# Kernel optimization log

Hardware: AMD Instinct MI355X
Metric: run time of the kernel (lower is better)

The kernel has to match this reference:

```python
import jax, jax.numpy as jnp
import numpy as np

N_NODES = 50000
N_EDGES = 800000
IN_DIM = 128
HID = 64
HEADS = 2
OUT_DIM = 2
N_GRAPHS = 512
NEG_SLOPE = 0.2


def setup_inputs() -> dict:
    key = jax.random.key(0)
    ks = jax.random.split(key, 16)
    x = jax.random.normal(ks[0], (N_NODES, IN_DIM), dtype=jnp.float32)
    edge_index = jax.random.randint(ks[1], (2, N_EDGES), 0, N_NODES, dtype=jnp.int64)
    batch = jnp.sort(jax.random.randint(ks[2], (N_NODES,), 0, N_GRAPHS, dtype=jnp.int64))
    s = 0.1
    W1 = jax.random.normal(ks[3], (IN_DIM, HEADS * HID), dtype=jnp.float32) * s
    a_src1 = jax.random.normal(ks[4], (HEADS, HID), dtype=jnp.float32) * s
    a_dst1 = jax.random.normal(ks[5], (HEADS, HID), dtype=jnp.float32) * s
    b1 = jnp.zeros((HEADS * HID,), dtype=jnp.float32)
    W2 = jax.random.normal(ks[6], (HEADS * HID, HID), dtype=jnp.float32) * s
    a_src2 = jax.random.normal(ks[7], (1, HID), dtype=jnp.float32) * s
    a_dst2 = jax.random.normal(ks[8], (1, HID), dtype=jnp.float32) * s
    b2 = jnp.zeros((HID,), dtype=jnp.float32)
    fcW = jax.random.normal(ks[9], (HID, OUT_DIM), dtype=jnp.float32) * s
    fcb = jnp.zeros((OUT_DIM,), dtype=jnp.float32)
    return dict(x=x, edge_index=edge_index, batch=batch,
                W1=W1, a_src1=a_src1, a_dst1=a_dst1, b1=b1,
                W2=W2, a_src2=a_src2, a_dst2=a_dst2, b2=b2,
                fcW=fcW, fcb=fcb)


def gat_layer(x, src, dst, W, a_src, a_dst, b, heads, c_out):
    # x: [N, F] -> h: [N, H, C]
    N = x.shape[0]
    h = (x @ W).reshape(N, heads, c_out)
    alpha_s = jnp.sum(h * a_src, axis=-1)  # [N, H]
    alpha_d = jnp.sum(h * a_dst, axis=-1)  # [N, H]
    e = jax.nn.leaky_relu(alpha_s[src] + alpha_d[dst], NEG_SLOPE)  # [E, H]
    # segment softmax over destination nodes
    emax = jax.ops.segment_max(e, dst, num_segments=N)  # [N, H]
    ex = jnp.exp(e - emax[dst])
    denom = jax.ops.segment_sum(ex, dst, num_segments=N)  # [N, H]
    coef = ex / denom[dst]  # [E, H]
    msg = h[src] * coef[..., None]  # [E, H, C]
    out = jax.ops.segment_sum(msg, dst, num_segments=N)  # [N, H, C]
    return out.reshape(N, heads * c_out) + b


def reference(x, edge_index, batch, W1, a_src1, a_dst1, b1, W2, a_src2, a_dst2, b2, fcW, fcb):
    N = x.shape[0]
    # PyG GATConv add_self_loops=True (shared graph for both layers)
    loops = jnp.arange(N, dtype=edge_index.dtype)
    src = jnp.concatenate([edge_index[0], loops])
    dst = jnp.concatenate([edge_index[1], loops])
    h = jax.nn.relu(gat_layer(x, src, dst, W1, a_src1, a_dst1, b1, HEADS, HID))
    h = jax.nn.relu(gat_layer(h, src, dst, W2, a_src2, a_dst2, b2, 1, HID))
    # global mean pool over graphs
    sums = jax.ops.segment_sum(h, batch, num_segments=N_GRAPHS)  # [G, HID]
    cnts = jax.ops.segment_sum(jnp.ones((N,), dtype=h.dtype), batch, num_segments=N_GRAPHS)
    pooled = sums / jnp.maximum(cnts, 1.0)[:, None]
    logits = pooled @ fcW + fcb
    return jax.nn.log_softmax(logits, axis=1)
```

## Files before the change

### kernel.cpp

```cpp
#include <hip/hip_runtime.h>
#include <math.h>

#define N_NODES 50000
#define N_EDGES 800000
#define EP (N_EDGES + N_NODES)
#define IN_DIM 128
#define HID 64
#define HEADS 2
#define OUT_DIM 2
#define N_GRAPHS 512
#define NEG_SLOPE 0.2f
#define NB_SCAN 196

typedef unsigned int uint;
typedef unsigned short ushort;

__device__ __forceinline__ ushort f2bf(float f) {
    uint u = __float_as_uint(f);
    u += 0x7fffu + ((u >> 16) & 1u);
    return (ushort)(u >> 16);
}
__device__ __forceinline__ float bf_lo(uint u) { return __uint_as_float(u << 16); }
__device__ __forceinline__ float bf_hi(uint u) { return __uint_as_float(u & 0xffff0000u); }

__global__ void hist_kernel(const int* __restrict__ ei, int* __restrict__ cnt) {
    int i = blockIdx.x * blockDim.x + threadIdx.x;
    if (i >= EP) return;
    int d = (i < N_EDGES) ? ei[N_EDGES + i] : (i - N_EDGES);
    atomicAdd(&cnt[d], 1);
}

__global__ void partial_kernel(const int* __restrict__ cnt, int* __restrict__ bsum) {
    int tid = threadIdx.x;
    int i = blockIdx.x * 256 + tid;
    int lane = tid & 63, wid = tid >> 6;
    int v = (i < N_NODES) ? cnt[i] : 0;
#pragma unroll
    for (int off = 32; off; off >>= 1) v += __shfl_xor(v, off);
    __shared__ int wsum[4];
    if (lane == 0) wsum[wid] = v;
    __syncthreads();
    if (tid == 0) bsum[blockIdx.x] = wsum[0] + wsum[1] + wsum[2] + wsum[3];
}

__global__ void scanb_kernel(const int* __restrict__ bsum, int* __restrict__ boff,
                             int* __restrict__ rowptr) {
    int tid = threadIdx.x;
    int lane = tid & 63, wid = tid >> 6;
    int v = (tid < NB_SCAN) ? bsum[tid] : 0;
    int incl = v;
#pragma unroll
    for (int off = 1; off < 64; off <<= 1) {
        int t = __shfl_up(incl, off);
        if (lane >= off) incl += t;
    }
    __shared__ int wt[4];
    if (lane == 63) wt[wid] = incl;
    __syncthreads();
    int add = 0;
    for (int w = 0; w < wid; w++) add += wt[w];
    incl += add;
    if (tid < NB_SCAN) boff[tid] = incl - v;
    if (tid == NB_SCAN - 1) rowptr[N_NODES] = incl;
}

__global__ void scanc_kernel(const int* __restrict__ cnt, const int* __restrict__ boff,
                             int* __restrict__ rowptr, int* __restrict__ cursor) {
    int tid = threadIdx.x;
    int i = blockIdx.x * 256 + tid;
    int lane = tid & 63, wid = tid >> 6;
    int v = (i < N_NODES) ? cnt[i] : 0;
    int incl = v;
#pragma unroll
    for (int off = 1; off < 64; off <<= 1) {
        int t = __shfl_up(incl, off);
        if (lane >= off) incl += t;
    }
    __shared__ int wt[4];
    if (lane == 63) wt[wid] = incl;
    __syncthreads();
    int add = boff[blockIdx.x];
    for (int w = 0; w < wid; w++) add += wt[w];
    int excl = add + incl - v;
    if (i < N_NODES) { rowptr[i] = excl; cursor[i] = excl; }
}

__global__ void scatter_kernel(const int* __restrict__ ei, int* __restrict__ cursor,
                               int* __restrict__ csr_src) {
    int i = blockIdx.x * blockDim.x + threadIdx.x;
    if (i >= EP) return;
    int s, d;
    if (i < N_EDGES) { s = ei[i]; d = ei[N_EDGES + i]; }
    else             { s = d = i - N_EDGES; }
    int pos = atomicAdd(&cursor[d], 1);
    csr_src[pos] = s;
}

template<int K, int COLS, int NPB>
__global__ void gemm_nodes(const float* __restrict__ X, const float* __restrict__ W,
                           ushort* __restrict__ Y, int n_nodes) {
    __shared__ float xs[NPB][K];
    const int base = blockIdx.x * NPB;
    const int tid = threadIdx.x;
    const float4* X4 = (const float4*)X;
    for (int idx = tid; idx < NPB * (K / 4); idx += COLS) {
        int r = idx / (K / 4), c = idx % (K / 4);
        int n = base + r;
        float4 v = (n < n_nodes) ? X4[(size_t)n * (K / 4) + c] : make_float4(0.f, 0.f, 0.f, 0.f);
        ((float4*)xs[r])[c] = v;
    }
    __syncthreads();
    float acc[NPB];
#pragma unroll
    for (int i = 0; i < NPB; i++) acc[i] = 0.f;
    for (int k = 0; k < K; k++) {
        float w = W[(size_t)k * COLS + tid];
#pragma unroll
        for (int i = 0; i < NPB; i++) acc[i] = fmaf(xs[i][k], w, acc[i]);
    }
#pragma unroll
    for (int i = 0; i < NPB; i++) {
        int n = base + i;
        if (n < n_nodes) Y[(size_t)n * COLS + tid] = f2bf(acc[i]);
    }
}

template<int H>
__global__ void alphas_kernel(const uint* __restrict__ Hb,
                              const float* __restrict__ a_src,
                              const float* __restrict__ a_dst,
                              float* __restrict__ as, float* __restrict__ ad, int n) {
    int i = blockIdx.x * blockDim.x + threadIdx.x;
    if (i >= n) return;
    const uint* hp = Hb + (size_t)i * (H * 32);
#pragma unroll
    for (int h = 0; h < H; h++) {
        float s = 0.f, d = 0.f;
#pragma unroll 8
        for (int j = 0; j < 32; j++) {
            uint u = hp[h * 32 + j];
            float v0 = bf_lo(u), v1 = bf_hi(u);
            s = fmaf(v0, a_src[h * 64 + 2 * j], s);
            s = fmaf(v1, a_src[h * 64 + 2 * j + 1], s);
            d = fmaf(v0, a_dst[h * 64 + 2 * j], d);
            d = fmaf(v1, a_dst[h * 64 + 2 * j + 1], d);
        }
        as[(size_t)i * H + h] = s;
        ad[(size_t)i * H + h] = d;
    }
}

__device__ __forceinline__ float lrelu(float e) { return e > 0.f ? e : NEG_SLOPE * e; }

__global__ void node_agg1_kernel(const int* __restrict__ rowptr, const int* __restrict__ csr_src,
                                 const uint* __restrict__ Hb,
                                 const float* __restrict__ as, const float* __restrict__ ad,
                                 const float* __restrict__ b, float* __restrict__ outp,
                                 float* __restrict__ exbuf) {
    int wave = threadIdx.x >> 6;
    int lane = threadIdx.x & 63;
    int node = blockIdx.x * 4 + wave;
    if (node >= N_NODES) return;
    const int lo = rowptr[node], hi = rowptr[node + 1];
    const float ad0 = ad[(size_t)node * 2 + 0], ad1 = ad[(size_t)node * 2 + 1];

    float d0 = 0.f, d1 = 0.f;
    for (int j = lo + lane; j < hi; j += 64) {
        int s = csr_src[j];
        float2 a = *(const float2*)&as[(size_t)s * 2];
        float ex0 = __expf(lrelu(a.x + ad0));
        float ex1 = __expf(lrelu(a.y + ad1));
        *(float2*)&exbuf[(size_t)j * 2] = make_float2(ex0, ex1);
        d0 += ex0; d1 += ex1;
    }
#pragma unroll
    for (int off = 32; off; off >>= 1) {
        d0 += __shfl_xor(d0, off);
        d1 += __shfl_xor(d1, off);
    }
    const float inv = (lane < 32) ? (1.f / d0) : (1.f / d1);

    float acc0 = 0.f, acc1 = 0.f;
    int j = lo;
    for (; j + 4 <= hi; j += 4) {
        int s0 = csr_src[j + 0], s1 = csr_src[j + 1];
        int s2 = csr_src[j + 2], s3 = csr_src[j + 3];
        float2 e0 = *(const float2*)&exbuf[(size_t)(j + 0) * 2];
        float2 e1 = *(const float2*)&exbuf[(size_t)(j + 1) * 2];
        float2 e2 = *(const float2*)&exbuf[(size_t)(j + 2) * 2];
        float2 e3 = *(const float2*)&exbuf[(size_t)(j + 3) * 2];
        uint u0 = Hb[(size_t)s0 * 64 + lane];
        uint u1 = Hb[(size_t)s1 * 64 + lane];
        uint u2 = Hb[(size_t)s2 * 64 + lane];
        uint u3 = Hb[(size_t)s3 * 64 + lane];
        float c0 = (lane < 32) ? e0.x : e0.y;
        float c1 = (lane < 32) ? e1.x : e1.y;
        float c2 = (lane < 32) ? e2.x : e2.y;
        float c3 = (lane < 32) ? e3.x : e3.y;
        acc0 = fmaf(bf_lo(u0), c0, acc0); acc1 = fmaf(bf_hi(u0), c0, acc1);
        acc0 = fmaf(bf_lo(u1), c1, acc0); acc1 = fmaf(bf_hi(u1), c1, acc1);
        acc0 = fmaf(bf_lo(u2), c2, acc0); acc1 = fmaf(bf_hi(u2), c2, acc1);
        acc0 = fmaf(bf_lo(u3), c3, acc0); acc1 = fmaf(bf_hi(u3), c3, acc1);
    }
    for (; j < hi; j++) {
        int s = csr_src[j];
        float2 e = *(const float2*)&exbuf[(size_t)j * 2];
        uint u = Hb[(size_t)s * 64 + lane];
        float c = (lane < 32) ? e.x : e.y;
        acc0 = fmaf(bf_lo(u), c, acc0);
        acc1 = fmaf(bf_hi(u), c, acc1);
    }
    float v0 = acc0 * inv + b[2 * lane];
    float v1 = acc1 * inv + b[2 * lane + 1];
    v0 = v0 > 0.f ? v0 : 0.f;
    v1 = v1 > 0.f ? v1 : 0.f;
    *(float2*)&outp[(size_t)node * 128 + 2 * lane] = make_float2(v0, v1);
}

__global__ void node_agg2_kernel(const int* __restrict__ rowptr, const int* __restrict__ csr_src,
                                 const ushort* __restrict__ Hb,
                                 const float* __restrict__ as, const float* __restrict__ ad,
                                 const float* __restrict__ b, float* __restrict__ outp,
                                 float* __restrict__ exbuf) {
    int wave = threadIdx.x >> 6;
    int lane = threadIdx.x & 63;
    int node = blockIdx.x * 4 + wave;
    if (node >= N_NODES) return;
    const int lo = rowptr[node], hi = rowptr[node + 1];
    const float adN = ad[node];

    float d = 0.f;
    for (int j = lo + lane; j < hi; j += 64) {
        float ex = __expf(lrelu(as[csr_src[j]] + adN));
        exbuf[j] = ex;
        d += ex;
    }
#pragma unroll
    for (int off = 32; off; off >>= 1) d += __shfl_xor(d, off);
    const float inv = 1.f / d;

    float acc = 0.f;
    int j = lo;
    for (; j + 4 <= hi; j += 4) {
        int s0 = csr_src[j + 0], s1 = csr_src[j + 1];
        int s2 = csr_src[j + 2], s3 = csr_src[j + 3];
        float e0 = exbuf[j + 0], e1 = exbuf[j + 1];
        float e2 = exbuf[j + 2], e3 = exbuf[j + 3];
        float h0 = __uint_as_float(((uint)Hb[(size_t)s0 * 64 + lane]) << 16);
        float h1 = __uint_as_float(((uint)Hb[(size_t)s1 * 64 + lane]) << 16);
        float h2 = __uint_as_float(((uint)Hb[(size_t)s2 * 64 + lane]) << 16);
        float h3 = __uint_as_float(((uint)Hb[(size_t)s3 * 64 + lane]) << 16);
        acc = fmaf(h0, e0, acc);
        acc = fmaf(h1, e1, acc);
        acc = fmaf(h2, e2, acc);
        acc = fmaf(h3, e3, acc);
    }
    for (; j < hi; j++)
        acc = fmaf(__uint_as_float(((uint)Hb[(size_t)csr_src[j] * 64 + lane]) << 16),
                   exbuf[j], acc);
    float v = acc * inv + b[lane];
    outp[(size_t)node * 64 + lane] = v > 0.f ? v : 0.f;
}

__global__ void pool_fc_kernel(const float* __restrict__ act2,
                               const int* __restrict__ batch,
                               const float* __restrict__ fcW,
                               const float* __restrict__ fcb,
                               float* __restrict__ out) {
    int g = blockIdx.x;
    int tid = threadIdx.x;
    int wid = tid >> 6, c = tid & 63;
    __shared__ int slo, shi;
    if (tid == 0) {
        int lo = 0, hi = N_NODES;
        while (lo < hi) { int m = (lo + hi) >> 1; if (batch[m] < g) lo = m + 1; else hi = m; }
        slo = lo;
        lo = 0; hi = N_NODES;
        while (lo < hi) { int m = (lo + hi) >> 1; if (batch[m] < g + 1) lo = m + 1; else hi = m; }
        shi = lo;
    }
    __syncthreads();
    const int lo = slo, hi = shi;
    float sum = 0.f;
    for (int n = lo + wid; n < hi; n += 4) sum += act2[(size_t)n * HID + c];
    __shared__ float ps[4][HID];
    ps[wid][c] = sum;
    __syncthreads();
    if (wid == 0) {
        float t = ps[0][c] + ps[1][c] + ps[2][c] + ps[3][c];
        float cnt = (float)(hi - lo);
        __shared__ float pooled[HID];
        pooled[c] = t / fmaxf(cnt, 1.f);
        __syncthreads();
        __shared__ float ls[OUT_DIM];
        if (c < OUT_DIM) {
            float l = fcb[c];
#pragma unroll 8
            for (int k = 0; k < HID; k++) l = fmaf(pooled[k], fcW[k * OUT_DIM + c], l);
            ls[c] = l;
        }
        __syncthreads();
        if (c < OUT_DIM) {
            float m = fmaxf(ls[0], ls[1]);
            float lse = m + logf(expf(ls[0] - m) + expf(ls[1] - m));
            out[(size_t)g * OUT_DIM + c] = ls[c] - lse;
        }
    }
}

extern "C" void kernel_launch(void* const* d_in, const int* in_sizes, int n_in,
                              void* d_out, int out_size, void* d_ws, size_t ws_size,
                              hipStream_t stream) {
    const float* x    = (const float*)d_in[0];
    const int*   ei   = (const int*)d_in[1];
    const int*   batch= (const int*)d_in[2];
    const float* W1   = (const float*)d_in[3];
    const float* as1w = (const float*)d_in[4];
    const float* ad1w = (const float*)d_in[5];
    const float* b1   = (const float*)d_in[6];
    const float* W2   = (const float*)d_in[7];
    const float* as2w = (const float*)d_in[8];
    const float* ad2w = (const float*)d_in[9];
    const float* b2   = (const float*)d_in[10];
    const float* fcW  = (const float*)d_in[11];
    const float* fcb  = (const float*)d_in[12];

    const size_t N = N_NODES;
    float* ws = (float*)d_ws;
    ushort* h1b  = (ushort*)ws;
    float* act1  = ws + N * 64;
    ushort* h2b  = (ushort*)(act1 + N * 128);
    float* out2  = act1 + N * 128 + N * 32;
    float* alps1 = out2 + N * 64;
    float* alpd1 = alps1 + N * 2;
    float* alps2 = alpd1 + N * 2;
    float* alpd2 = alps2 + N;
    int* cnt     = (int*)(alpd2 + N);
    int* rowptr  = cnt + N;
    int* cursor  = rowptr + N + 1;
    int* bsum    = cursor + N;
    int* boff    = bsum + NB_SCAN;
    int* csr_src = boff + NB_SCAN;
    float* exbuf = (float*)(csr_src + EP);

    hipMemsetAsync(cnt, 0, N * sizeof(int), stream);
    hist_kernel<<<(EP + 255) / 256, 256, 0, stream>>>(ei, cnt);
    partial_kernel<<<NB_SCAN, 256, 0, stream>>>(cnt, bsum);
    scanb_kernel<<<1, 256, 0, stream>>>(bsum, boff, rowptr);
    scanc_kernel<<<NB_SCAN, 256, 0, stream>>>(cnt, boff, rowptr, cursor);
    scatter_kernel<<<(EP + 255) / 256, 256, 0, stream>>>(ei, cursor, csr_src);

    gemm_nodes<128, 128, 4><<<(N + 3) / 4, 128, 0, stream>>>(x, W1, h1b, (int)N);
    alphas_kernel<2><<<(N + 255) / 256, 256, 0, stream>>>((const uint*)h1b, as1w, ad1w, alps1, alpd1, (int)N);
    node_agg1_kernel<<<(N + 3) / 4, 256, 0, stream>>>(rowptr, csr_src, (const uint*)h1b, alps1, alpd1, b1, act1, exbuf);

    gemm_nodes<128, 64, 8><<<(N + 7) / 8, 64, 0, stream>>>(act1, W2, h2b, (int)N);
    alphas_kernel<1><<<(N + 255) / 256, 256, 0, stream>>>((const uint*)h2b, as2w, ad2w, alps2, alpd2, (int)N);
    node_agg2_kernel<<<(N + 3) / 4, 256, 0, stream>>>(rowptr, csr_src, h2b, alps2, alpd2, b2, out2, exbuf);

    pool_fc_kernel<<<N_GRAPHS, 256, 0, stream>>>(out2, batch, fcW, fcb, (float*)d_out);
}
```

Measured before the change: 355.5 us.

## Fuse attention-logit dot products into GEMM and keep edge exps in registers

The separate alphas kernels are folded into the node GEMM: each wave multiplies its fp32 accumulators by a_src/a_dst and reduces them with a wave shuffle, so the bf16 features are not read back and two launches disappear. In both aggregation kernels the per-edge exp values are no longer written to and re-read from a global exbuf. For the first 128 edges of each node they stay in registers and are broadcast with __shfl, and edges beyond 128 recompute the exp. The alphas now come from unrounded fp32 accumulators rather than bf16 values, which slightly changes numerics. The GEMM epilogue gains a shuffle reduction per node.

```diff
diff --git a/kernel.cpp b/kernel.cpp
--- a/kernel.cpp
+++ b/kernel.cpp
@@ -96,12 +96,15 @@
     csr_src[pos] = s;
 }
 
-template<int K, int COLS, int NPB>
-__global__ void gemm_nodes(const float* __restrict__ X, const float* __restrict__ W,
-                           ushort* __restrict__ Y, int n_nodes) {
+template<int K, int COLS, int NPB, int H>
+__global__ void gemm_alphas(const float* __restrict__ X, const float* __restrict__ W,
+                            ushort* __restrict__ Y,
+                            const float* __restrict__ a_src, const float* __restrict__ a_dst,
+                            float* __restrict__ as, float* __restrict__ ad, int n_nodes) {
     __shared__ float xs[NPB][K];
     const int base = blockIdx.x * NPB;
     const int tid = threadIdx.x;
+    const int lane = tid & 63, wid = tid >> 6;
     const float4* X4 = (const float4*)X;
     for (int idx = tid; idx < NPB * (K / 4); idx += COLS) {
         int r = idx / (K / 4), c = idx % (K / 4);
@@ -110,6 +113,8 @@
         ((float4*)xs[r])[c] = v;
     }
     __syncthreads();
+    const float asv = a_src[wid * 64 + lane];
+    const float adv = a_dst[wid * 64 + lane];
     float acc[NPB];
 #pragma unroll
     for (int i = 0; i < NPB; i++) acc[i] = 0.f;
@@ -121,32 +126,19 @@
 #pragma unroll
     for (int i = 0; i < NPB; i++) {
         int n = base + i;
-        if (n < n_nodes) Y[(size_t)n * COLS + tid] = f2bf(acc[i]);
-    }
-}
-
-template<int H>
-__global__ void alphas_kernel(const uint* __restrict__ Hb,
-                              const float* __restrict__ a_src,
-                              const float* __restrict__ a_dst,
-                              float* __restrict__ as, float* __restrict__ ad, int n) {
-    int i = blockIdx.x * blockDim.x + threadIdx.x;
-    if (i >= n) return;
-    const uint* hp = Hb + (size_t)i * (H * 32);
-#pragma unroll
-    for (int h = 0; h < H; h++) {
-        float s = 0.f, d = 0.f;
-#pragma unroll 8
-        for (int j = 0; j < 32; j++) {
-            uint u = hp[h * 32 + j];
-            float v0 = bf_lo(u), v1 = bf_hi(u);
-            s = fmaf(v0, a_src[h * 64 + 2 * j], s);
-            s = fmaf(v1, a_src[h * 64 + 2 * j + 1], s);
-            d = fmaf(v0, a_dst[h * 64 + 2 * j], d);
-            d = fmaf(v1, a_dst[h * 64 + 2 * j + 1], d);
-        }
-        as[(size_t)i * H + h] = s;
-        ad[(size_t)i * H + h] = d;
+        if (n >= n_nodes) continue;
+        Y[(size_t)n * COLS + tid] = f2bf(acc[i]);
+        float s = acc[i] * asv;
+        float d = acc[i] * adv;
+#pragma unroll
+        for (int off = 32; off; off >>= 1) {
+            s += __shfl_xor(s, off);
+            d += __shfl_xor(d, off);
+        }
+        if (lane == 0) {
+            as[(size_t)n * H + wid] = s;
+            ad[(size_t)n * H + wid] = d;
+        }
     }
 }
 
@@ -155,8 +147,7 @@
 __global__ void node_agg1_kernel(const int* __restrict__ rowptr, const int* __restrict__ csr_src,
                                  const uint* __restrict__ Hb,
                                  const float* __restrict__ as, const float* __restrict__ ad,
-                                 const float* __restrict__ b, float* __restrict__ outp,
-                                 float* __restrict__ exbuf) {
+                                 const float* __restrict__ b, float* __restrict__ outp) {
     int wave = threadIdx.x >> 6;
     int lane = threadIdx.x & 63;
     int node = blockIdx.x * 4 + wave;
@@ -164,14 +155,27 @@
     const int lo = rowptr[node], hi = rowptr[node + 1];
     const float ad0 = ad[(size_t)node * 2 + 0], ad1 = ad[(size_t)node * 2 + 1];
 
-    float d0 = 0.f, d1 = 0.f;
-    for (int j = lo + lane; j < hi; j += 64) {
+    float exa0 = 0.f, exa1 = 0.f, exb0 = 0.f, exb1 = 0.f;
+    int j1 = lo + lane;
+    if (j1 < hi) {
+        int s = csr_src[j1];
+        float2 a = *(const float2*)&as[(size_t)s * 2];
+        exa0 = __expf(lrelu(a.x + ad0));
+        exa1 = __expf(lrelu(a.y + ad1));
+    }
+    int j2 = lo + 64 + lane;
+    if (j2 < hi) {
+        int s = csr_src[j2];
+        float2 a = *(const float2*)&as[(size_t)s * 2];
+        exb0 = __expf(lrelu(a.x + ad0));
+        exb1 = __expf(lrelu(a.y + ad1));
+    }
+    float d0 = exa0 + exb0, d1 = exa1 + exb1;
+    for (int j = lo + 128 + lane; j < hi; j += 64) {
         int s = csr_src[j];
         float2 a = *(const float2*)&as[(size_t)s * 2];
-        float ex0 = __expf(lrelu(a.x + ad0));
-        float ex1 = __expf(lrelu(a.y + ad1));
-        *(float2*)&exbuf[(size_t)j * 2] = make_float2(ex0, ex1);
-        d0 += ex0; d1 += ex1;
+        d0 += __expf(lrelu(a.x + ad0));
+        d1 += __expf(lrelu(a.y + ad1));
     }
 #pragma unroll
     for (int off = 32; off; off >>= 1) {
@@ -179,36 +183,60 @@
         d1 += __shfl_xor(d1, off);
     }
     const float inv = (lane < 32) ? (1.f / d0) : (1.f / d1);
+    const bool h0side = (lane < 32);
 
     float acc0 = 0.f, acc1 = 0.f;
-    int j = lo;
-    for (; j + 4 <= hi; j += 4) {
-        int s0 = csr_src[j + 0], s1 = csr_src[j + 1];
-        int s2 = csr_src[j + 2], s3 = csr_src[j + 3];
-        float2 e0 = *(const float2*)&exbuf[(size_t)(j + 0) * 2];
-        float2 e1 = *(const float2*)&exbuf[(size_t)(j + 1) * 2];
-        float2 e2 = *(const float2*)&exbuf[(size_t)(j + 2) * 2];
-        float2 e3 = *(const float2*)&exbuf[(size_t)(j + 3) * 2];
+    const int deg = hi - lo;
+    const int n1 = deg < 64 ? deg : 64;
+    int j = 0;
+    for (; j + 4 <= n1; j += 4) {
+        int s0 = csr_src[lo + j + 0], s1 = csr_src[lo + j + 1];
+        int s2 = csr_src[lo + j + 2], s3 = csr_src[lo + j + 3];
+        float ca0 = __shfl(exa0, j + 0), cb0 = __shfl(exa1, j + 0);
+        float ca1 = __shfl(exa0, j + 1), cb1 = __shfl(exa1, j + 1);
+        float ca2 = __shfl(exa0, j + 2), cb2 = __shfl(exa1, j + 2);
+        float ca3 = __shfl(exa0, j + 3), cb3 = __shfl(exa1, j + 3);
+        float c0 = h0side ? ca0 : cb0;
+        float c1 = h0side ? ca1 : cb1;
+        float c2 = h0side ? ca2 : cb2;
+        float c3 = h0side ? ca3 : cb3;
         uint u0 = Hb[(size_t)s0 * 64 + lane];
         uint u1 = Hb[(size_t)s1 * 64 + lane];
         uint u2 = Hb[(size_t)s2 * 64 + lane];
         uint u3 = Hb[(size_t)s3 * 64 + lane];
-        float c0 = (lane < 32) ? e0.x : e0.y;
-        float c1 = (lane < 32) ? e1.x : e1.y;
-        float c2 = (lane < 32) ? e2.x : e2.y;
-        float c3 = (lane < 32) ? e3.x : e3.y;
         acc0 = fmaf(bf_lo(u0), c0, acc0); acc1 = fmaf(bf_hi(u0), c0, acc1);
         acc0 = fmaf(bf_lo(u1), c1, acc0); acc1 = fmaf(bf_hi(u1), c1, acc1);
         acc0 = fmaf(bf_lo(u2), c2, acc0); acc1 = fmaf(bf_hi(u2), c2, acc1);
         acc0 = fmaf(bf_lo(u3), c3, acc0); acc1 = fmaf(bf_hi(u3), c3, acc1);
     }
-    for (; j < hi; j++) {
-        int s = csr_src[j];
-        float2 e = *(const float2*)&exbuf[(size_t)j * 2];
+    for (; j < n1; j++) {
+        int s = csr_src[lo + j];
+        float ca = __shfl(exa0, j), cb = __shfl(exa1, j);
+        float c = h0side ? ca : cb;
         uint u = Hb[(size_t)s * 64 + lane];
-        float c = (lane < 32) ? e.x : e.y;
         acc0 = fmaf(bf_lo(u), c, acc0);
         acc1 = fmaf(bf_hi(u), c, acc1);
+    }
+    if (deg > 64) {
+        const int n2 = deg < 128 ? deg : 128;
+        for (j = 64; j < n2; j++) {
+            int s = csr_src[lo + j];
+            float ca = __shfl(exb0, j - 64), cb = __shfl(exb1, j - 64);
+            float c = h0side ? ca : cb;
+            uint u = Hb[(size_t)s * 64 + lane];
+            acc0 = fmaf(bf_lo(u), c, acc0);
+            acc1 = fmaf(bf_hi(u), c, acc1);
+        }
+        for (int jj = lo + 128; jj < hi; jj++) {
+            int s = csr_src[jj];
+            float2 a = *(const float2*)&as[(size_t)s * 2];
+            float e0 = __expf(lrelu(a.x + ad0));
+            float e1 = __expf(lrelu(a.y + ad1));
+            float c = h0side ? e0 : e1;
+            uint u = Hb[(size_t)s * 64 + lane];
+            acc0 = fmaf(bf_lo(u), c, acc0);
+            acc1 = fmaf(bf_hi(u), c, acc1);
+        }
     }
     float v0 = acc0 * inv + b[2 * lane];
     float v1 = acc1 * inv + b[2 * lane + 1];
@@ -220,8 +248,7 @@
 __global__ void node_agg2_kernel(const int* __restrict__ rowptr, const int* __restrict__ csr_src,
                                  const ushort* __restrict__ Hb,
                                  const float* __restrict__ as, const float* __restrict__ ad,
-                                 const float* __restrict__ b, float* __restrict__ outp,
-                                 float* __restrict__ exbuf) {
+                                 const float* __restrict__ b, float* __restrict__ outp) {
     int wave = threadIdx.x >> 6;
     int lane = threadIdx.x & 63;
     int node = blockIdx.x * 4 + wave;
@@ -229,35 +256,52 @@
     const int lo = rowptr[node], hi = rowptr[node + 1];
     const float adN = ad[node];
 
-    float d = 0.f;
-    for (int j = lo + lane; j < hi; j += 64) {
-        float ex = __expf(lrelu(as[csr_src[j]] + adN));
-        exbuf[j] = ex;
-        d += ex;
-    }
+    float exa = 0.f, exb = 0.f;
+    int j1 = lo + lane;
+    if (j1 < hi) exa = __expf(lrelu(as[csr_src[j1]] + adN));
+    int j2 = lo + 64 + lane;
+    if (j2 < hi) exb = __expf(lrelu(as[csr_src[j2]] + adN));
+    float d = exa + exb;
+    for (int j = lo + 128 + lane; j < hi; j += 64)
+        d += __expf(lrelu(as[csr_src[j]] + adN));
 #pragma unroll
     for (int off = 32; off; off >>= 1) d += __shfl_xor(d, off);
     const float inv = 1.f / d;
 
     float acc = 0.f;
-    int j = lo;
-    for (; j + 4 <= hi; j += 4) {
-        int s0 = csr_src[j + 0], s1 = csr_src[j + 1];
-        int s2 = csr_src[j + 2], s3 = csr_src[j + 3];
-        float e0 = exbuf[j + 0], e1 = exbuf[j + 1];
-        float e2 = exbuf[j + 2], e3 = exbuf[j + 3];
+    const int deg = hi - lo;
+    const int n1 = deg < 64 ? deg : 64;
+    int j = 0;
+    for (; j + 4 <= n1; j += 4) {
+        int s0 = csr_src[lo + j + 0], s1 = csr_src[lo + j + 1];
+        int s2 = csr_src[lo + j + 2], s3 = csr_src[lo + j + 3];
+        float c0 = __shfl(exa, j + 0), c1 = __shfl(exa, j + 1);
+        float c2 = __shfl(exa, j + 2), c3 = __shfl(exa, j + 3);
         float h0 = __uint_as_float(((uint)Hb[(size_t)s0 * 64 + lane]) << 16);
         float h1 = __uint_as_float(((uint)Hb[(size_t)s1 * 64 + lane]) << 16);
         float h2 = __uint_as_float(((uint)Hb[(size_t)s2 * 64 + lane]) << 16);
         float h3 = __uint_as_float(((uint)Hb[(size_t)s3 * 64 + lane]) << 16);
-        acc = fmaf(h0, e0, acc);
-        acc = fmaf(h1, e1, acc);
-        acc = fmaf(h2, e2, acc);
-        acc = fmaf(h3, e3, acc);
-    }
-    for (; j < hi; j++)
-        acc = fmaf(__uint_as_float(((uint)Hb[(size_t)csr_src[j] * 64 + lane]) << 16),
-                   exbuf[j], acc);
+        acc = fmaf(h0, c0, acc);
+        acc = fmaf(h1, c1, acc);
+        acc = fmaf(h2, c2, acc);
+        acc = fmaf(h3, c3, acc);
+    }
+    for (; j < n1; j++) {
+        float c = __shfl(exa, j);
+        acc = fmaf(__uint_as_float(((uint)Hb[(size_t)csr_src[lo + j] * 64 + lane]) << 16), c, acc);
+    }
+    if (deg > 64) {
+        const int n2 = deg < 128 ? deg : 128;
+        for (j = 64; j < n2; j++) {
+            float c = __shfl(exb, j - 64);
+            acc = fmaf(__uint_as_float(((uint)Hb[(size_t)csr_src[lo + j] * 64 + lane]) << 16), c, acc);
+        }
+        for (int jj = lo + 128; jj < hi; jj++) {
+            int s = csr_src[jj];
+            float c = __expf(lrelu(as[s] + adN));
+            acc = fmaf(__uint_as_float(((uint)Hb[(size_t)s * 64 + lane]) << 16), c, acc);
+        }
+    }
     float v = acc * inv + b[lane];
     outp[(size_t)node * 64 + lane] = v > 0.f ? v : 0.f;
 }
@@ -341,7 +385,6 @@
     int* bsum    = cursor + N;
     int* boff    = bsum + NB_SCAN;
     int* csr_src = boff + NB_SCAN;
-    float* exbuf = (float*)(csr_src + EP);
 
     hipMemsetAsync(cnt, 0, N * sizeof(int), stream);
     hist_kernel<<<(EP + 255) / 256, 256, 0, stream>>>(ei, cnt);
@@ -350,13 +393,15 @@
     scanc_kernel<<<NB_SCAN, 256, 0, stream>>>(cnt, boff, rowptr, cursor);
     scatter_kernel<<<(EP + 255) / 256, 256, 0, stream>>>(ei, cursor, csr_src);
 
-    gemm_nodes<128, 128, 4><<<(N + 3) / 4, 128, 0, stream>>>(x, W1, h1b, (int)N);
-    alphas_kernel<2><<<(N + 255) / 256, 256, 0, stream>>>((const uint*)h1b, as1w, ad1w, alps1, alpd1, (int)N);
-    node_agg1_kernel<<<(N + 3) / 4, 256, 0, stream>>>(rowptr, csr_src, (const uint*)h1b, alps1, alpd1, b1, act1, exbuf);
-
-    gemm_nodes<128, 64, 8><<<(N + 7) / 8, 64, 0, stream>>>(act1, W2, h2b, (int)N);
-    alphas_kernel<1><<<(N + 255) / 256, 256, 0, stream>>>((const uint*)h2b, as2w, ad2w, alps2, alpd2, (int)N);
-    node_agg2_kernel<<<(N + 3) / 4, 256, 0, stream>>>(rowptr, csr_src, h2b, alps2, alpd2, b2, out2, exbuf);
+    gemm_alphas<128, 128, 4, 2><<<(N + 3) / 4, 128, 0, stream>>>(
+        x, W1, h1b, as1w, ad1w, alps1, alpd1, (int)N);
+    node_agg1_kernel<<<(N + 3) / 4, 256, 0, stream>>>(
+        rowptr, csr_src, (const uint*)h1b, alps1, alpd1, b1, act1);
+
+    gemm_alphas<128, 64, 8, 1><<<(N + 7) / 8, 64, 0, stream>>>(
+        act1, W2, h2b, as2w, ad2w, alps2, alpd2, (int)N);
+    node_agg2_kernel<<<(N + 3) / 4, 256, 0, stream>>>(
+        rowptr, csr_src, h2b, alps2, alpd2, b2, out2);
 
     pool_fc_kernel<<<N_GRAPHS, 256, 0, stream>>>(out2, batch, fcW, fcb, (float*)d_out);
 }
```

Measured after the change: 351.1 us. No clear change (-1.2%).
